# Kernel optimization log

Measured on AMD Instinct MI355X. Metric: run time of the kernel, lower is better.

Reference implementation:

```python
import jax, jax.numpy as jnp
import numpy as np

D_MODEL = 1024
H = 16
D_K = D_MODEL // H


def setup_inputs() -> dict:
    key = jax.random.key(0)
    ks = jax.random.split(key, 11)
    B, S = 4, 2048
    q = jax.random.normal(ks[0], (B, S, D_MODEL), dtype=jnp.float32)
    k = jax.random.normal(ks[1], (B, S, D_MODEL), dtype=jnp.float32)
    v = jax.random.normal(ks[2], (B, S, D_MODEL), dtype=jnp.float32)
    mask = jnp.ones((1, 1, S, S), dtype=bool)  # all-ones = no masking
    scale = 1.0 / np.sqrt(D_MODEL)
    wq = jax.random.normal(ks[3], (D_MODEL, D_MODEL), dtype=jnp.float32) * scale
    wk = jax.random.normal(ks[4], (D_MODEL, D_MODEL), dtype=jnp.float32) * scale
    wv = jax.random.normal(ks[5], (D_MODEL, D_MODEL), dtype=jnp.float32) * scale
    wo = jax.random.normal(ks[6], (D_MODEL, D_MODEL), dtype=jnp.float32) * scale
    bq = jnp.zeros((D_MODEL,), jnp.float32)
    bk = jnp.zeros((D_MODEL,), jnp.float32)
    bv = jnp.zeros((D_MODEL,), jnp.float32)
    bo = jnp.zeros((D_MODEL,), jnp.float32)
    return {"q": q, "k": k, "v": v, "mask": mask,
            "wq": wq, "bq": bq, "wk": wk, "bk": bk,
            "wv": wv, "bv": bv, "wo": wo, "bo": bo}


def reference(q, k, v, mask, wq, bq, wk, bk, wv, bv, wo, bo):
    B, S, _ = q.shape
    # projections (Linear uses x @ W^T + b)
    qh = (q @ wq.T + bq).reshape(B, S, H, D_K).transpose(0, 2, 1, 3)  # [B,H,S,Dk]
    kh = (k @ wk.T + bk).reshape(B, S, H, D_K).transpose(0, 2, 1, 3)
    vh = (v @ wv.T + bv).reshape(B, S, H, D_K).transpose(0, 2, 1, 3)
    scores = jnp.einsum("bhqd,bhkd->bhqk", qh, kh) / jnp.sqrt(jnp.float32(D_K))
    scores = jnp.where(mask, scores, jnp.float32(-1e9))
    attn = jax.nn.softmax(scores, axis=-1)  # dropout p=0.0 -> identity
    out = jnp.einsum("bhqk,bhkd->bhqd", attn, vh)  # [B,H,S,Dk]
    out = out.transpose(0, 2, 1, 3).reshape(B, S, D_MODEL)
    return out @ wo.T + bo
```

## Files before the change

### kernel.cpp

```cpp
#include <hip/hip_runtime.h>
#include <hip/hip_bf16.h>


typedef __attribute__((ext_vector_type(8))) short bf16x8;
typedef __attribute__((ext_vector_type(4))) float f32x4;
typedef __attribute__((ext_vector_type(16))) float f32x16;

__device__ __forceinline__ float fast_exp2(float x) {
  return __builtin_amdgcn_exp2f(x);
}

__device__ __forceinline__ void gload_lds16(const void* g, void* l) {
  __builtin_amdgcn_global_load_lds(
      (const __attribute__((address_space(1))) unsigned int*)g,
      (__attribute__((address_space(3))) unsigned int*)l, 16, 0, 0);
}

__global__ void cvt_bf16_multi(const float* __restrict__ s0, const float* __restrict__ s1,
                               const float* __restrict__ s2, const float* __restrict__ s3,
                               __hip_bfloat16* __restrict__ d0, __hip_bfloat16* __restrict__ d1,
                               __hip_bfloat16* __restrict__ d2, __hip_bfloat16* __restrict__ d3,
                               int n4) {
  const int z = blockIdx.y;
  const float* in = (z == 0) ? s0 : (z == 1) ? s1 : (z == 2) ? s2 : s3;
  __hip_bfloat16* out = (z == 0) ? d0 : (z == 1) ? d1 : (z == 2) ? d2 : d3;
  int stride = gridDim.x * blockDim.x;
  for (int i = blockIdx.x * blockDim.x + threadIdx.x; i < n4; i += stride) {
    float4 f = reinterpret_cast<const float4*>(in)[i];
    union { __hip_bfloat16 h[4]; ushort4 u; } cv;
    cv.h[0] = __float2bfloat16(f.x);
    cv.h[1] = __float2bfloat16(f.y);
    cv.h[2] = __float2bfloat16(f.z);
    cv.h[3] = __float2bfloat16(f.w);
    reinterpret_cast<ushort4*>(out)[i] = cv.u;
  }
}

template <int MODE>
__device__ __forceinline__ void gemm_tile(const __hip_bfloat16* __restrict__ A,
                                          const __hip_bfloat16* __restrict__ W,
                                          const float* __restrict__ bias,
                                          void* __restrict__ out, float scale,
                                          int m0, int n0,
                                          __hip_bfloat16* As, __hip_bfloat16* Bs) {
  const int t = threadIdx.x;
  const int lane = t & 63;
  const int w = t >> 6;
  const int lrow = lane & 15, lk = lane >> 4;
  const int wr = (w >> 1) << 6;
  const int wc = (w & 1) << 6;
  const int K = 1024, N = 1024;

  f32x4 acc[4][4] = {};
  const char* Ab = (const char*)As;
  const char* Bb = (const char*)Bs;

  for (int kt = 0; kt < K; kt += 64) {
    #pragma unroll
    for (int j = 0; j < 4; ++j) {
      int i = j * 256 + t;
      int row = i >> 3;
      int cs = ((i & 7) ^ (row & 7)) << 3;
      gload_lds16(A + (size_t)(m0 + row) * K + kt + cs, (char*)As + (i << 4));
      gload_lds16(W + (size_t)(n0 + row) * K + kt + cs, (char*)Bs + (i << 4));
    }
    __syncthreads();
    #pragma unroll
    for (int h = 0; h < 2; ++h) {
      bf16x8 a[4], b[4];
      #pragma unroll
      for (int f = 0; f < 4; ++f) {
        const int sw = ((h * 4 + lk) ^ (lrow & 7)) << 4;
        a[f] = *(const bf16x8*)(Ab + (wr + f * 16 + lrow) * 128 + sw);
        b[f] = *(const bf16x8*)(Bb + (wc + f * 16 + lrow) * 128 + sw);
      }
      #pragma unroll
      for (int fi = 0; fi < 4; ++fi)
        #pragma unroll
        for (int fj = 0; fj < 4; ++fj)
          acc[fi][fj] = __builtin_amdgcn_mfma_f32_16x16x32_bf16(a[fi], b[fj], acc[fi][fj], 0, 0, 0);
    }
    __syncthreads();
  }

  #pragma unroll
  for (int fi = 0; fi < 4; ++fi) {
    int rbase = m0 + wr + fi * 16 + (lk << 2);
    #pragma unroll
    for (int fj = 0; fj < 4; ++fj) {
      int gc = n0 + wc + fj * 16 + lrow;
      float bv = bias[gc];
      #pragma unroll
      for (int r = 0; r < 4; ++r) {
        int gm = rbase + r;
        float val = (acc[fi][fj][r] + bv) * scale;
        if (MODE == 0) {
          int bb = gm >> 11, ss = gm & 2047, hh = gc >> 6, dd = gc & 63;
          ((__hip_bfloat16*)out)[((((size_t)bb * 16 + hh) * 2048 + ss) << 6) + dd] =
              __float2bfloat16(val);
        } else {
          ((float*)out)[(size_t)gm * N + gc] = val;
        }
      }
    }
  }
}

__global__ __launch_bounds__(256, 3)
void gemm_qkv_kernel(const __hip_bfloat16* __restrict__ A0, const __hip_bfloat16* __restrict__ A1,
                     const __hip_bfloat16* __restrict__ A2,
                     const __hip_bfloat16* __restrict__ W0, const __hip_bfloat16* __restrict__ W1,
                     const __hip_bfloat16* __restrict__ W2,
                     const float* __restrict__ b0, const float* __restrict__ b1,
                     const float* __restrict__ b2,
                     __hip_bfloat16* __restrict__ o0, __hip_bfloat16* __restrict__ o1,
                     __hip_bfloat16* __restrict__ o2,
                     float sc0, float sc1, float sc2) {
  __shared__ __hip_bfloat16 As[128 * 64];
  __shared__ __hip_bfloat16 Bs[128 * 64];
  const int flat = blockIdx.x;
  const int swz = (flat & 7) * 192 + (flat >> 3);
  const int z = swz >> 9;
  const int rem = swz & 511;
  const int m0 = (rem >> 3) << 7;
  const int n0 = (rem & 7) << 7;
  const __hip_bfloat16* A = A0; const __hip_bfloat16* W = W0;
  const float* bias = b0; __hip_bfloat16* out = o0; float scale = sc0;
  if (z == 1) { A = A1; W = W1; bias = b1; out = o1; scale = sc1; }
  else if (z == 2) { A = A2; W = W2; bias = b2; out = o2; scale = sc2; }
  gemm_tile<0>(A, W, bias, out, scale, m0, n0, As, Bs);
}

__global__ __launch_bounds__(256, 3)
void gemm_out_kernel(const __hip_bfloat16* __restrict__ A, const __hip_bfloat16* __restrict__ W,
                     const float* __restrict__ bias, float* __restrict__ out) {
  __shared__ __hip_bfloat16 As[128 * 64];
  __shared__ __hip_bfloat16 Bs[128 * 64];
  const int flat = blockIdx.x;
  const int swz = (flat & 7) * 64 + (flat >> 3);
  const int m0 = (swz >> 3) << 7;
  const int n0 = (swz & 7) << 7;
  gemm_tile<1>(A, W, bias, out, 1.0f, m0, n0, As, Bs);
}


template <int OFF>
__device__ __forceinline__ bf16x8 pack8(const f32x16& v) {
  bf16x8 r;
  #pragma unroll
  for (int e = 0; e < 8; ++e) {
    union { __hip_bfloat16 h; short s; } u;
    u.h = __float2bfloat16(v[OFF + e]);
    r[e] = u.s;
  }
  return r;
}

__global__ __launch_bounds__(512, 4)
void attn32_kernel(const __hip_bfloat16* __restrict__ qh,
                   const __hip_bfloat16* __restrict__ kh,
                   const __hip_bfloat16* __restrict__ vh,
                   __hip_bfloat16* __restrict__ att) {
  const int t = threadIdx.x;
  const int lane = t & 63, w = t >> 6;
  const int l31 = lane & 31, g = lane >> 5;
  const int bh = blockIdx.x, q0 = blockIdx.y << 8;

  const __hip_bfloat16* Qp = qh + (size_t)bh * 2048 * 64;
  const __hip_bfloat16* Kp = kh + (size_t)bh * 2048 * 64;
  const __hip_bfloat16* Vp = vh + (size_t)bh * 2048 * 64;

  __shared__ __align__(16) char lds[2 * 8192 + 2 * 9216];

  const int qrow = q0 + w * 32 + l31;
  bf16x8 bq[4];
  #pragma unroll
  for (int ks = 0; ks < 4; ++ks)
    bq[ks] = *(const bf16x8*)(Qp + (size_t)qrow * 64 + ks * 16 + g * 8);

  f32x16 o0 = {}, o1 = {};
  float m_run = -1e30f, l_run = 0.f;

  const int krow = t >> 3, kcc = t & 7;
  const size_t kgo = (size_t)krow * 64 + ((kcc ^ (krow & 7)) << 3);
  const int klo = t << 4;
  const int vkey = t & 63, vdb = w << 3;
  const size_t vgo = (size_t)vkey * 64 + vdb;
  const int kpos = (vkey & 0x30) | (vkey & 3) | ((vkey & 4) << 1) | ((vkey & 8) >> 1);
  int ka[4], kb_[4], va_[4], vb_[4];
  #pragma unroll
  for (int ks = 0; ks < 4; ++ks) {
    ka[ks] = l31 * 128 + (((ks * 2 + g) ^ (l31 & 7)) << 4);
    kb_[ks] = ka[ks] + 32 * 128;
  }
  #pragma unroll
  for (int st = 0; st < 4; ++st) {
    va_[st] = l31 * 144 + st * 32 + g * 16;
    vb_[st] = va_[st] + 32 * 144;
  }

  auto vwrite = [&](char* Vn, const bf16x8& v) {
    #pragma unroll
    for (int e = 0; e < 8; ++e)
      *(unsigned short*)(Vn + (vdb + e) * 144 + kpos * 2) = (unsigned short)v[e];
  };

  {
    gload_lds16(Kp + kgo, lds + klo);
    bf16x8 v0 = *(const bf16x8*)(Vp + vgo);
    vwrite(lds + 16384, v0);
  }
  __syncthreads();

  for (int kt = 0; kt < 32; ++kt) {
    const int cur = kt & 1;
    const char* Kc = lds + (cur ? 8192 : 0);
    const char* Vc = lds + 16384 + (cur ? 9216 : 0);
    char* Kn = lds + (cur ? 0 : 8192);
    char* Vn = lds + 16384 + (cur ? 0 : 9216);

    bf16x8 vr;
    const bool pre = (kt < 31);
    if (pre) {
      const size_t k0n = (size_t)(kt + 1) * 64 * 64;
      gload_lds16(Kp + k0n + kgo, Kn + klo);
      vr = *(const bf16x8*)(Vp + k0n + vgo);
    }

    f32x16 s0 = {}, s1 = {};
    __builtin_amdgcn_s_setprio(1);
    #pragma unroll
    for (int ks = 0; ks < 4; ++ks) {
      bf16x8 a0 = *(const bf16x8*)(Kc + ka[ks]);
      bf16x8 a1 = *(const bf16x8*)(Kc + kb_[ks]);
      s0 = __builtin_amdgcn_mfma_f32_32x32x16_bf16(a0, bq[ks], s0, 0, 0, 0);
      s1 = __builtin_amdgcn_mfma_f32_32x32x16_bf16(a1, bq[ks], s1, 0, 0, 0);
    }
    __builtin_amdgcn_s_setprio(0);

    float mx[8];
    #pragma unroll
    for (int j = 0; j < 8; ++j)
      mx[j] = fmaxf(fmaxf(s0[j], s0[j + 8]), fmaxf(s1[j], s1[j + 8]));
    float tm = fmaxf(fmaxf(fmaxf(mx[0], mx[1]), fmaxf(mx[2], mx[3])),
                     fmaxf(fmaxf(mx[4], mx[5]), fmaxf(mx[6], mx[7])));
    tm = fmaxf(tm, __shfl_xor(tm, 32));
    if (!__all(tm <= m_run + 11.5416f)) {
      float mn = fmaxf(m_run, tm);
      float sc = fast_exp2(m_run - mn);
      m_run = mn; l_run *= sc;
      #pragma unroll
      for (int j = 0; j < 16; ++j) { o0[j] *= sc; o1[j] *= sc; }
    }
    #pragma unroll
    for (int j = 0; j < 16; ++j) {
      s0[j] = fast_exp2(s0[j] - m_run);
      s1[j] = fast_exp2(s1[j] - m_run);
    }
    float as[8];
    #pragma unroll
    for (int j = 0; j < 8; ++j) as[j] = (s0[j] + s0[j + 8]) + (s1[j] + s1[j + 8]);
    float ps = ((as[0] + as[1]) + (as[2] + as[3])) + ((as[4] + as[5]) + (as[6] + as[7]));
    ps += __shfl_xor(ps, 32);
    l_run += ps;

    bf16x8 pb0 = pack8<0>(s0), pb1 = pack8<8>(s0);
    bf16x8 pb2 = pack8<0>(s1), pb3 = pack8<8>(s1);

    __builtin_amdgcn_s_setprio(1);
    #pragma unroll
    for (int st = 0; st < 4; ++st) {
      bf16x8 av0 = *(const bf16x8*)(Vc + va_[st]);
      bf16x8 av1 = *(const bf16x8*)(Vc + vb_[st]);
      const bf16x8 pb = (st == 0) ? pb0 : (st == 1) ? pb1 : (st == 2) ? pb2 : pb3;
      o0 = __builtin_amdgcn_mfma_f32_32x32x16_bf16(av0, pb, o0, 0, 0, 0);
      o1 = __builtin_amdgcn_mfma_f32_32x32x16_bf16(av1, pb, o1, 0, 0, 0);
    }
    __builtin_amdgcn_s_setprio(0);

    if (pre) vwrite(Vn, vr);
    __syncthreads();
  }

  const int bb = bh >> 4, hh = bh & 15;
  const float inv = 1.f / l_run;
  __hip_bfloat16* obase = att + ((size_t)bb * 2048 + qrow) * 1024 + hh * 64 + g * 16;

  auto epi = [&](const f32x16& acc, __hip_bfloat16* dst) {
    float fin[16];
    #pragma unroll
    for (int c2 = 0; c2 < 2; ++c2)
      #pragma unroll
      for (int c4 = 0; c4 < 4; ++c4) {
        float sendv = g ? acc[c4 + 4 * c2] : acc[c4 + 4 * (2 + c2)];
        float recvv = __shfl_xor(sendv, 32);
        float ownv  = g ? acc[c4 + 4 * (2 + c2)] : acc[c4 + 4 * c2];
        fin[c2 * 8 + c4]     = g ? recvv : ownv;
        fin[c2 * 8 + 4 + c4] = g ? ownv : recvv;
      }
    bf16x8 w0, w1;
    #pragma unroll
    for (int j = 0; j < 8; ++j) {
      union { __hip_bfloat16 h; short s; } u0, u1;
      u0.h = __float2bfloat16(fin[j] * inv);
      u1.h = __float2bfloat16(fin[8 + j] * inv);
      w0[j] = u0.s; w1[j] = u1.s;
    }
    *(bf16x8*)dst = w0;
    *(bf16x8*)(dst + 8) = w1;
  };
  epi(o0, obase);
  epi(o1, obase + 32);
}

extern "C" void kernel_launch(void* const* d_in, const int* in_sizes, int n_in,
                              void* d_out, int out_size, void* d_ws, size_t ws_size,
                              hipStream_t stream) {
  (void)in_sizes; (void)n_in; (void)out_size; (void)ws_size;
  const float* q  = (const float*)d_in[0];
  const float* k  = (const float*)d_in[1];
  const float* v  = (const float*)d_in[2];
  const float* wq = (const float*)d_in[4];
  const float* bq = (const float*)d_in[5];
  const float* wk = (const float*)d_in[6];
  const float* bk = (const float*)d_in[7];
  const float* wv = (const float*)d_in[8];
  const float* bv = (const float*)d_in[9];
  const float* wo = (const float*)d_in[10];
  const float* bo = (const float*)d_in[11];

  char* ws = (char*)d_ws;
  const size_t MB = 1u << 20;
  __hip_bfloat16* qb   = (__hip_bfloat16*)(ws);
  __hip_bfloat16* kb   = (__hip_bfloat16*)(ws + 16 * MB);
  __hip_bfloat16* vb   = (__hip_bfloat16*)(ws + 32 * MB);
  __hip_bfloat16* wqb  = (__hip_bfloat16*)(ws + 48 * MB);
  __hip_bfloat16* wkb  = (__hip_bfloat16*)(ws + 50 * MB);
  __hip_bfloat16* wvb  = (__hip_bfloat16*)(ws + 52 * MB);
  __hip_bfloat16* wob  = (__hip_bfloat16*)(ws + 54 * MB);
  __hip_bfloat16* qhb  = (__hip_bfloat16*)(ws + 56 * MB);
  __hip_bfloat16* khb  = (__hip_bfloat16*)(ws + 72 * MB);
  __hip_bfloat16* vhb  = (__hip_bfloat16*)(ws + 88 * MB);
  __hip_bfloat16* attb = qb;

  dim3 blk(256);
  const int nw4 = (1024 * 1024) / 4;
  const int nx4 = (4 * 2048 * 1024) / 4;
  const float qscale = 0.125f * 1.44269504f;

  cvt_bf16_multi<<<dim3(256, 4), blk, 0, stream>>>(wq, wk, wv, wo,
                                                   wqb, wkb, wvb, wob, nw4);
  cvt_bf16_multi<<<dim3(1024, 3), blk, 0, stream>>>(q, k, v, nullptr,
                                                    qb, kb, vb, nullptr, nx4);

  gemm_qkv_kernel<<<dim3(1536), blk, 0, stream>>>(qb, kb, vb, wqb, wkb, wvb,
                                                  bq, bk, bv, qhb, khb, vhb,
                                                  qscale, 1.0f, 1.0f);

  attn32_kernel<<<dim3(64, 8), dim3(512), 0, stream>>>(qhb, khb, vhb, attb);

  gemm_out_kernel<<<dim3(512), blk, 0, stream>>>(attb, wob, bo, (float*)d_out);
}
```

Measured before the change: 204.8 us.

## Fuse fp32-to-bf16 activation conversion into QKV GEMM and double attention K/V tile

The QKV projection GEMM now reads the fp32 q/k/v activations directly and converts them to bf16 while staging into LDS, so the separate conversion kernel and its bf16 intermediate buffers are gone. This removes a full read and write pass over the activations, but the A operand now goes through registers instead of direct global-to-LDS loads. Separately, the attention kernel processes two 64-key subtiles per barrier iteration with four-way LDS buffering, halving the number of synchronisations. That doubles LDS usage, which may lower occupancy.

```diff
diff --git a/kernel.cpp b/kernel.cpp
--- a/kernel.cpp
+++ b/kernel.cpp
@@ -36,8 +36,8 @@
   }
 }
 
-template <int MODE>
-__device__ __forceinline__ void gemm_tile(const __hip_bfloat16* __restrict__ A,
+template <int MODE, int ASRC>
+__device__ __forceinline__ void gemm_tile(const void* Av,
                                           const __hip_bfloat16* __restrict__ W,
                                           const float* __restrict__ bias,
                                           void* __restrict__ out, float scale,
@@ -61,8 +61,32 @@
       int i = j * 256 + t;
       int row = i >> 3;
       int cs = ((i & 7) ^ (row & 7)) << 3;
-      gload_lds16(A + (size_t)(m0 + row) * K + kt + cs, (char*)As + (i << 4));
       gload_lds16(W + (size_t)(n0 + row) * K + kt + cs, (char*)Bs + (i << 4));
+      if (ASRC == 0)
+        gload_lds16((const __hip_bfloat16*)Av + (size_t)(m0 + row) * K + kt + cs,
+                    (char*)As + (i << 4));
+    }
+    if (ASRC == 1) {
+      const float* A32 = (const float*)Av;
+      #pragma unroll
+      for (int j = 0; j < 4; ++j) {
+        int i = j * 256 + t;
+        int row = i >> 3;
+        int cs = ((i & 7) ^ (row & 7)) << 3;
+        const float* src = A32 + (size_t)(m0 + row) * K + kt + cs;
+        float4 f0 = *(const float4*)src;
+        float4 f1 = *(const float4*)(src + 4);
+        union { __hip_bfloat16 h[8]; bf16x8 v; } cv;
+        cv.h[0] = __float2bfloat16(f0.x);
+        cv.h[1] = __float2bfloat16(f0.y);
+        cv.h[2] = __float2bfloat16(f0.z);
+        cv.h[3] = __float2bfloat16(f0.w);
+        cv.h[4] = __float2bfloat16(f1.x);
+        cv.h[5] = __float2bfloat16(f1.y);
+        cv.h[6] = __float2bfloat16(f1.z);
+        cv.h[7] = __float2bfloat16(f1.w);
+        *(bf16x8*)((char*)As + (i << 4)) = cv.v;
+      }
     }
     __syncthreads();
     #pragma unroll
@@ -107,8 +131,8 @@
 }
 
 __global__ __launch_bounds__(256, 3)
-void gemm_qkv_kernel(const __hip_bfloat16* __restrict__ A0, const __hip_bfloat16* __restrict__ A1,
-                     const __hip_bfloat16* __restrict__ A2,
+void gemm_qkv_kernel(const float* __restrict__ A0, const float* __restrict__ A1,
+                     const float* __restrict__ A2,
                      const __hip_bfloat16* __restrict__ W0, const __hip_bfloat16* __restrict__ W1,
                      const __hip_bfloat16* __restrict__ W2,
                      const float* __restrict__ b0, const float* __restrict__ b1,
@@ -124,11 +148,11 @@
   const int rem = swz & 511;
   const int m0 = (rem >> 3) << 7;
   const int n0 = (rem & 7) << 7;
-  const __hip_bfloat16* A = A0; const __hip_bfloat16* W = W0;
+  const float* A = A0; const __hip_bfloat16* W = W0;
   const float* bias = b0; __hip_bfloat16* out = o0; float scale = sc0;
   if (z == 1) { A = A1; W = W1; bias = b1; out = o1; scale = sc1; }
   else if (z == 2) { A = A2; W = W2; bias = b2; out = o2; scale = sc2; }
-  gemm_tile<0>(A, W, bias, out, scale, m0, n0, As, Bs);
+  gemm_tile<0, 1>(A, W, bias, out, scale, m0, n0, As, Bs);
 }
 
 __global__ __launch_bounds__(256, 3)
@@ -140,7 +164,7 @@
   const int swz = (flat & 7) * 64 + (flat >> 3);
   const int m0 = (swz >> 3) << 7;
   const int n0 = (swz & 7) << 7;
-  gemm_tile<1>(A, W, bias, out, 1.0f, m0, n0, As, Bs);
+  gemm_tile<1, 0>(A, W, bias, out, 1.0f, m0, n0, As, Bs);
 }
 
 
@@ -170,7 +194,8 @@
   const __hip_bfloat16* Kp = kh + (size_t)bh * 2048 * 64;
   const __hip_bfloat16* Vp = vh + (size_t)bh * 2048 * 64;
 
-  __shared__ __align__(16) char lds[2 * 8192 + 2 * 9216];
+  __shared__ __align__(16) char lds[4 * 8192 + 4 * 9216];
+  char* const Vbase = lds + 4 * 8192;
 
   const int qrow = q0 + w * 32 + l31;
   bf16x8 bq[4];
@@ -184,7 +209,7 @@
   const int krow = t >> 3, kcc = t & 7;
   const size_t kgo = (size_t)krow * 64 + ((kcc ^ (krow & 7)) << 3);
   const int klo = t << 4;
-  const int vkey = t & 63, vdb = w << 3;
+  const int vkey = t & 63, vdb = (t >> 6) << 3;
   const size_t vgo = (size_t)vkey * 64 + vdb;
   const int kpos = (vkey & 0x30) | (vkey & 3) | ((vkey & 4) << 1) | ((vkey & 8) >> 1);
   int ka[4], kb_[4], va_[4], vb_[4];
@@ -205,28 +230,7 @@
       *(unsigned short*)(Vn + (vdb + e) * 144 + kpos * 2) = (unsigned short)v[e];
   };
 
-  {
-    gload_lds16(Kp + kgo, lds + klo);
-    bf16x8 v0 = *(const bf16x8*)(Vp + vgo);
-    vwrite(lds + 16384, v0);
-  }
-  __syncthreads();
-
-  for (int kt = 0; kt < 32; ++kt) {
-    const int cur = kt & 1;
-    const char* Kc = lds + (cur ? 8192 : 0);
-    const char* Vc = lds + 16384 + (cur ? 9216 : 0);
-    char* Kn = lds + (cur ? 0 : 8192);
-    char* Vn = lds + 16384 + (cur ? 0 : 9216);
-
-    bf16x8 vr;
-    const bool pre = (kt < 31);
-    if (pre) {
-      const size_t k0n = (size_t)(kt + 1) * 64 * 64;
-      gload_lds16(Kp + k0n + kgo, Kn + klo);
-      vr = *(const bf16x8*)(Vp + k0n + vgo);
-    }
-
+  auto subtile = [&](const char* Kc, const char* Vc) {
     f32x16 s0 = {}, s1 = {};
     __builtin_amdgcn_s_setprio(1);
     #pragma unroll
@@ -277,8 +281,44 @@
       o1 = __builtin_amdgcn_mfma_f32_32x32x16_bf16(av1, pb, o1, 0, 0, 0);
     }
     __builtin_amdgcn_s_setprio(0);
-
-    if (pre) vwrite(Vn, vr);
+  };
+
+  {
+    #pragma unroll
+    for (int s = 0; s < 2; ++s) {
+      gload_lds16(Kp + s * 4096 + kgo, lds + s * 8192 + klo);
+      bf16x8 v0 = *(const bf16x8*)(Vp + s * 4096 + vgo);
+      vwrite(Vbase + s * 9216, v0);
+    }
+  }
+  __syncthreads();
+
+  for (int it = 0; it < 16; ++it) {
+    const int P = it & 1;
+    const char* Kc0 = lds + (P * 2) * 8192;
+    const char* Kc1 = Kc0 + 8192;
+    const char* Vc0 = Vbase + (P * 2) * 9216;
+    const char* Vc1 = Vc0 + 9216;
+    char* Kn0 = lds + ((P ^ 1) * 2) * 8192;
+    char* Vn0 = Vbase + ((P ^ 1) * 2) * 9216;
+
+    bf16x8 vrA, vrB;
+    const bool pre = (it < 15);
+    if (pre) {
+      const size_t nb = (size_t)(it + 1) * 8192;
+      gload_lds16(Kp + nb + kgo, Kn0 + klo);
+      gload_lds16(Kp + nb + 4096 + kgo, Kn0 + 8192 + klo);
+      vrA = *(const bf16x8*)(Vp + nb + vgo);
+      vrB = *(const bf16x8*)(Vp + nb + 4096 + vgo);
+    }
+
+    subtile(Kc0, Vc0);
+    subtile(Kc1, Vc1);
+
+    if (pre) {
+      vwrite(Vn0, vrA);
+      vwrite(Vn0 + 9216, vrB);
+    }
     __syncthreads();
   }
 
@@ -331,29 +371,23 @@
 
   char* ws = (char*)d_ws;
   const size_t MB = 1u << 20;
-  __hip_bfloat16* qb   = (__hip_bfloat16*)(ws);
-  __hip_bfloat16* kb   = (__hip_bfloat16*)(ws + 16 * MB);
-  __hip_bfloat16* vb   = (__hip_bfloat16*)(ws + 32 * MB);
-  __hip_bfloat16* wqb  = (__hip_bfloat16*)(ws + 48 * MB);
-  __hip_bfloat16* wkb  = (__hip_bfloat16*)(ws + 50 * MB);
-  __hip_bfloat16* wvb  = (__hip_bfloat16*)(ws + 52 * MB);
-  __hip_bfloat16* wob  = (__hip_bfloat16*)(ws + 54 * MB);
-  __hip_bfloat16* qhb  = (__hip_bfloat16*)(ws + 56 * MB);
-  __hip_bfloat16* khb  = (__hip_bfloat16*)(ws + 72 * MB);
-  __hip_bfloat16* vhb  = (__hip_bfloat16*)(ws + 88 * MB);
-  __hip_bfloat16* attb = qb;
+  __hip_bfloat16* wqb  = (__hip_bfloat16*)(ws);
+  __hip_bfloat16* wkb  = (__hip_bfloat16*)(ws + 2 * MB);
+  __hip_bfloat16* wvb  = (__hip_bfloat16*)(ws + 4 * MB);
+  __hip_bfloat16* wob  = (__hip_bfloat16*)(ws + 6 * MB);
+  __hip_bfloat16* qhb  = (__hip_bfloat16*)(ws + 8 * MB);
+  __hip_bfloat16* khb  = (__hip_bfloat16*)(ws + 24 * MB);
+  __hip_bfloat16* vhb  = (__hip_bfloat16*)(ws + 40 * MB);
+  __hip_bfloat16* attb = (__hip_bfloat16*)(ws + 56 * MB);
 
   dim3 blk(256);
   const int nw4 = (1024 * 1024) / 4;
-  const int nx4 = (4 * 2048 * 1024) / 4;
   const float qscale = 0.125f * 1.44269504f;
 
   cvt_bf16_multi<<<dim3(256, 4), blk, 0, stream>>>(wq, wk, wv, wo,
                                                    wqb, wkb, wvb, wob, nw4);
-  cvt_bf16_multi<<<dim3(1024, 3), blk, 0, stream>>>(q, k, v, nullptr,
-                                                    qb, kb, vb, nullptr, nx4);
-
-  gemm_qkv_kernel<<<dim3(1536), blk, 0, stream>>>(qb, kb, vb, wqb, wkb, wvb,
+
+  gemm_qkv_kernel<<<dim3(1536), blk, 0, stream>>>(q, k, v, wqb, wkb, wvb,
                                                   bq, bk, bv, qhb, khb, vhb,
                                                   qscale, 1.0f, 1.0f);
 
```

Measured after the change: 193.2 us. 5.7% less time.
